# Optimization experiments

Hardware: AMD Instinct MI355X
Metric: run time of the kernel (lower is better)

## Reference

```python
import jax, jax.numpy as jnp
import numpy as np

HIDDEN = 1024
HEADS = 16
HEAD_DIM = HIDDEN // HEADS  # 64
LOCAL = (128, 128)
ROPE_MAX_POS = LOCAL[0] + LOCAL[1]  # 256 (local attention branch)
ROPE_BASE = 10000.0


def make_rope_cache(max_len, dim, base):
    positions = jnp.arange(max_len, dtype=jnp.float32)
    theta = 1.0 / base ** (jnp.arange(0, dim, 2, dtype=jnp.float32) / dim)
    angles = jnp.einsum('i,j->ij', positions, theta)
    return jnp.stack([jnp.cos(angles), jnp.sin(angles)], axis=-1)  # (max_len, dim//2, 2)


def apply_rope(x, cache):
    # x: (B, S, H, D); cache: (max_pos, D//2, 2)
    S = x.shape[1]
    pos = jnp.arange(S) % cache.shape[0]
    rc = cache[pos][None, :, None, :, :]  # (1, S, 1, D//2, 2)
    xr = x.reshape(*x.shape[:-1], -1, 2)
    x0, x1 = xr[..., 0], xr[..., 1]
    c, s = rc[..., 0], rc[..., 1]
    out = jnp.stack([x0 * c - x1 * s, x1 * c + x0 * s], axis=-1)
    return out.reshape(x.shape)


def sliding_window_mask(S, window, dtype):
    rel = jnp.arange(S)[:, None] - jnp.arange(S)[None, :]
    inside = (rel >= -window[0]) & (rel <= window[1])
    return jnp.where(inside, jnp.zeros((), dtype), -jnp.inf)[None, None]  # (1,1,S,S)


def setup_inputs() -> dict:
    key = jax.random.key(0)
    k1, k2, k3, k4, k5 = jax.random.split(key, 5)
    B, S = 2, 2048
    hidden_states = jax.random.normal(k1, (B, S, HIDDEN), dtype=jnp.float32)
    Wqkv_kernel = jax.random.normal(k2, (HIDDEN, 3 * HIDDEN), dtype=jnp.float32) / np.sqrt(HIDDEN)
    Wqkv_bias = jnp.zeros((3 * HIDDEN,), dtype=jnp.float32)
    Wo_kernel = jax.random.normal(k3, (HIDDEN, HIDDEN), dtype=jnp.float32) / np.sqrt(HIDDEN)
    Wo_bias = jnp.zeros((HIDDEN,), dtype=jnp.float32)
    rope_cache = make_rope_cache(ROPE_MAX_POS, HEAD_DIM, ROPE_BASE)
    return {
        'hidden_states': hidden_states,
        'Wqkv_kernel': Wqkv_kernel,
        'Wqkv_bias': Wqkv_bias,
        'Wo_kernel': Wo_kernel,
        'Wo_bias': Wo_bias,
        'rope_cache': rope_cache,
    }


def reference(hidden_states, Wqkv_kernel, Wqkv_bias, Wo_kernel, Wo_bias, rope_cache):
    B, S, _ = hidden_states.shape
    qkv = hidden_states @ Wqkv_kernel + Wqkv_bias  # (B,S,3*HIDDEN)
    qkv = qkv.reshape(B, S, 3, HEADS, HEAD_DIM)
    q = qkv[:, :, 0]  # (B,S,H,D)
    k = qkv[:, :, 1]
    v = qkv[:, :, 2]
    q = apply_rope(q, rope_cache)
    k = apply_rope(k, rope_cache)
    # to (B,H,S,D)
    q = jnp.transpose(q, (0, 2, 1, 3))
    k = jnp.transpose(k, (0, 2, 1, 3))
    v = jnp.transpose(v, (0, 2, 1, 3))
    scale = jnp.sqrt(jnp.float32(HEAD_DIM))
    scores = jnp.einsum('bhqd,bhkd->bhqk', q, k) / scale
    mask = sliding_window_mask(S, LOCAL, scores.dtype)
    probs = jax.nn.softmax(scores + mask, axis=-1)
    out = jnp.einsum('bhqk,bhkd->bqhd', probs, v).reshape(B, S, HIDDEN)
    out = out @ Wo_kernel + Wo_bias
    return out
```

## Files before the change

kernel.cpp:

```cpp
#include <hip/hip_runtime.h>
#include <hip/hip_bf16.h>

typedef __bf16 bf16x8 __attribute__((ext_vector_type(8)));
typedef __bf16 bf16x4 __attribute__((ext_vector_type(4)));
typedef float f32x4 __attribute__((ext_vector_type(4)));

#define SLEN 2048
#define NHEADS 16
#define HDIM 64

__global__ __launch_bounds__(256) void prep(const float* __restrict__ hidden,
                                            const float* __restrict__ Wqkv,
                                            const float* __restrict__ Wo,
                                            __bf16* __restrict__ A1,
                                            __bf16* __restrict__ Wt,
                                            __bf16* __restrict__ Wot) {
    int b = blockIdx.x;
    if (b < 4096) {
        int i = b * 256 + threadIdx.x;
        float4 v = reinterpret_cast<const float4*>(hidden)[i];
        bf16x4 o = { (__bf16)v.x, (__bf16)v.y, (__bf16)v.z, (__bf16)v.w };
        reinterpret_cast<bf16x4*>(A1)[i] = o;
    } else {
        __shared__ float tile[32][33];
        const float* W; __bf16* Dst; int N, bx, by;
        if (b < 7168) { int bb = b - 4096; W = Wqkv; Dst = Wt;  N = 3072; bx = bb % 96; by = bb / 96; }
        else          { int bb = b - 7168; W = Wo;   Dst = Wot; N = 1024; bx = bb % 32; by = bb / 32; }
        int tx = threadIdx.x & 31, ty = threadIdx.x >> 5;
        int n0 = bx * 32, k0 = by * 32;
        #pragma unroll
        for (int i = ty; i < 32; i += 8)
            tile[i][tx] = W[(size_t)(k0 + i) * N + n0 + tx];
        __syncthreads();
        #pragma unroll
        for (int i = ty; i < 32; i += 8)
            Dst[(size_t)(n0 + i) * 1024 + k0 + tx] = (__bf16)tile[tx][i];
    }
}

template <int TN>
__global__ __launch_bounds__(256) void gemm_bt(const __bf16* __restrict__ A,
                                               const __bf16* __restrict__ Bt,
                                               const float* __restrict__ bias,
                                               float* __restrict__ Cf,
                                               __bf16* __restrict__ Cq,
                                               __bf16* __restrict__ Ck,
                                               __bf16* __restrict__ Cv,
                                               int M, int N, int K, int epi) {
    constexpr int JN = TN / 32;
    __shared__ __align__(16) __bf16 As[128 * 40];
    __shared__ __align__(16) __bf16 Bs[TN * 40];

    int nb = N / TN;
    int bx = blockIdx.x % nb;
    int by = blockIdx.x / nb;
    int row0 = by * 128, col0 = bx * TN;

    int tid = threadIdx.x;
    int wave = tid >> 6, lane = tid & 63;
    int quad = lane >> 4, lrow = lane & 15;
    int wm = wave >> 1, wn = wave & 1;

    int r1 = tid >> 2;
    int kk = (tid & 3) * 8;
    const __bf16* Aptr = A + (size_t)(row0 + r1) * K + kk;
    const __bf16* Bptr = Bt + (size_t)(col0 + r1) * K + kk;

    f32x4 acc[4][JN];
    f32x4 zero = {0.f, 0.f, 0.f, 0.f};
    #pragma unroll
    for (int i = 0; i < 4; i++)
        #pragma unroll
        for (int j = 0; j < JN; j++) acc[i][j] = zero;

    for (int k0 = 0; k0 < K; k0 += 32) {
        bf16x8 a0 = *reinterpret_cast<const bf16x8*>(Aptr + k0);
        bf16x8 a1 = *reinterpret_cast<const bf16x8*>(Aptr + (size_t)64 * K + k0);
        bf16x8 b0 = *reinterpret_cast<const bf16x8*>(Bptr + k0);
        bf16x8 b1;
        if (TN == 128) b1 = *reinterpret_cast<const bf16x8*>(Bptr + (size_t)64 * K + k0);
        __syncthreads();
        *reinterpret_cast<bf16x8*>(&As[r1 * 40 + kk]) = a0;
        *reinterpret_cast<bf16x8*>(&As[(r1 + 64) * 40 + kk]) = a1;
        *reinterpret_cast<bf16x8*>(&Bs[r1 * 40 + kk]) = b0;
        if (TN == 128) *reinterpret_cast<bf16x8*>(&Bs[(r1 + 64) * 40 + kk]) = b1;
        __syncthreads();

        bf16x8 af[4], bfr[JN];
        #pragma unroll
        for (int i = 0; i < 4; i++)
            af[i] = *reinterpret_cast<const bf16x8*>(&As[(wm * 64 + i * 16 + lrow) * 40 + quad * 8]);
        #pragma unroll
        for (int j = 0; j < JN; j++)
            bfr[j] = *reinterpret_cast<const bf16x8*>(&Bs[(wn * (TN / 2) + j * 16 + lrow) * 40 + quad * 8]);
        #pragma unroll
        for (int i = 0; i < 4; i++)
            #pragma unroll
            for (int j = 0; j < JN; j++)
                acc[i][j] = __builtin_amdgcn_mfma_f32_16x16x32_bf16(af[i], bfr[j], acc[i][j], 0, 0, 0);
    }

    int part = col0 >> 10;
    #pragma unroll
    for (int i = 0; i < 4; i++) {
        int rowb = row0 + wm * 64 + i * 16 + quad * 4;
        #pragma unroll
        for (int j = 0; j < JN; j++) {
            int col = col0 + wn * (TN / 2) + j * 16 + lrow;
            float bsv = bias[col];
            #pragma unroll
            for (int r = 0; r < 4; r++) {
                int row = rowb + r;
                float v = acc[i][j][r] + bsv;
                if (epi == 0) {
                    Cf[(size_t)row * N + col] = v;
                } else {
                    int h = (col >> 6) & 15;
                    int d = col & 63;
                    int b = row >> 11;
                    int s = row & 2047;
                    __bf16* dst = (part == 0) ? Cq : ((part == 1) ? Ck : Cv);
                    dst[((size_t)(b * NHEADS + h) * SLEN + s) * HDIM + d] = (__bf16)v;
                }
            }
        }
    }
}

__global__ __launch_bounds__(256) void rope_kernel(__bf16* __restrict__ Q,
                                                   __bf16* __restrict__ K,
                                                   const float* __restrict__ rope) {
    int idx = blockIdx.x * 256 + threadIdx.x;
    int p = idx & 31;
    int s = (idx >> 5) & 2047;
    int bh = idx >> 16;
    size_t off = ((size_t)bh * SLEN + s) * HDIM + 2 * p;
    int pos = s & 255;
    float c = rope[(pos * 32 + p) * 2];
    float sn = rope[(pos * 32 + p) * 2 + 1];
    float q0 = (float)Q[off], q1 = (float)Q[off + 1];
    Q[off]     = (__bf16)(q0 * c - q1 * sn);
    Q[off + 1] = (__bf16)(q1 * c + q0 * sn);
    float k0 = (float)K[off], k1 = (float)K[off + 1];
    K[off]     = (__bf16)(k0 * c - k1 * sn);
    K[off + 1] = (__bf16)(k1 * c + k0 * sn);
}

__global__ __launch_bounds__(256) void attn_kernel(const __bf16* __restrict__ Q,
                                                   const __bf16* __restrict__ K,
                                                   const __bf16* __restrict__ V,
                                                   __bf16* __restrict__ O) {
    __shared__ __align__(16) __bf16 Vt[64][328];
    __shared__ __align__(16) __bf16 Pl[4][16][40];

    int qt = blockIdx.x & 31;
    int bh = blockIdx.x >> 5;
    int q0 = qt * 64;
    int kbase0 = q0 - 128;
    const __bf16* Qbh = Q + (size_t)bh * SLEN * HDIM;
    const __bf16* Kbh = K + (size_t)bh * SLEN * HDIM;
    const __bf16* Vbh = V + (size_t)bh * SLEN * HDIM;

    int tid = threadIdx.x;
    int wave = tid >> 6, lane = tid & 63;
    int quad = lane >> 4, lrow = lane & 15;
    int wq0 = q0 + wave * 16;

    {
        int dchunk = wave * 16;
        #pragma unroll
        for (int k = 0; k < 5; k++) {
            int off = k * 64 + lane;
            int krow = kbase0 + off;
            krow = min(max(krow, 0), SLEN - 1);
            const __bf16* vp = Vbh + (size_t)krow * HDIM + dchunk;
            bf16x8 v0 = *reinterpret_cast<const bf16x8*>(vp);
            bf16x8 v1 = *reinterpret_cast<const bf16x8*>(vp + 8);
            #pragma unroll
            for (int i = 0; i < 8; i++) {
                Vt[dchunk + i][off] = v0[i];
                Vt[dchunk + 8 + i][off] = v1[i];
            }
        }
    }

    bf16x8 qb0 = *reinterpret_cast<const bf16x8*>(Qbh + (size_t)(wq0 + lrow) * HDIM + quad * 8);
    bf16x8 qb1 = *reinterpret_cast<const bf16x8*>(Qbh + (size_t)(wq0 + lrow) * HDIM + 32 + quad * 8);

    __syncthreads();

    f32x4 zero = {0.f, 0.f, 0.f, 0.f};
    f32x4 acc[4], acc_l = zero;
    #pragma unroll
    for (int t = 0; t < 4; t++) acc[t] = zero;

    bf16x8 ones = { (__bf16)1.f, (__bf16)1.f, (__bf16)1.f, (__bf16)1.f,
                    (__bf16)1.f, (__bf16)1.f, (__bf16)1.f, (__bf16)1.f };

    int cbeg = wave >> 1;
    if (q0 < 128) { int e = (128 - q0) >> 5; if (e > cbeg) cbeg = e; }
    int cend = (16 * wave + 271) >> 5;
    { int e = (2175 - q0) >> 5; if (e < cend) cend = e; }

    auto loadK = [&](int c, bf16x8 kf[2][2]) {
        int kb = kbase0 + c * 32;
        #pragma unroll
        for (int sub = 0; sub < 2; sub++) {
            int kr = kb + sub * 16 + lrow;
            int krc = min(max(kr, 0), SLEN - 1);
            const __bf16* kp = Kbh + (size_t)krc * HDIM;
            kf[sub][0] = *reinterpret_cast<const bf16x8*>(kp + quad * 8);
            kf[sub][1] = *reinterpret_cast<const bf16x8*>(kp + 32 + quad * 8);
        }
    };

    bf16x8 ka[2][2];
    loadK(cbeg, ka);

    for (int c = cbeg; c <= cend; c++) {
        bf16x8 kn[2][2];
        if (c < cend) loadK(c + 1, kn);

        int kb = kbase0 + c * 32;
        int loc = c * 32;

        f32x4 st[2];
        #pragma unroll
        for (int sub = 0; sub < 2; sub++) {
            st[sub] = __builtin_amdgcn_mfma_f32_16x16x32_bf16(ka[sub][0], qb0, zero, 0, 0, 0);
            st[sub] = __builtin_amdgcn_mfma_f32_16x16x32_bf16(ka[sub][1], qb1, st[sub], 0, 0, 0);
        }

        int q = wq0 + lrow;
        #pragma unroll
        for (int sub = 0; sub < 2; sub++) {
            bf16x4 pk;
            #pragma unroll
            for (int r = 0; r < 4; r++) {
                int key = kb + sub * 16 + quad * 4 + r;
                int rel = key - q;
                bool valid = (rel >= -128) && (rel <= 128) && (key >= 0) && (key < SLEN);
                float p = valid ? __expf(st[sub][r] * 0.125f) : 0.0f;
                pk[r] = (__bf16)p;
            }
            *reinterpret_cast<bf16x4*>(&Pl[wave][lrow][sub * 16 + quad * 4]) = pk;
        }
        asm volatile("s_waitcnt lgkmcnt(0)" ::: "memory");

        bf16x8 bp = *reinterpret_cast<const bf16x8*>(&Pl[wave][lrow][quad * 8]);
        acc_l = __builtin_amdgcn_mfma_f32_16x16x32_bf16(ones, bp, acc_l, 0, 0, 0);
        #pragma unroll
        for (int t = 0; t < 4; t++) {
            bf16x8 va = *reinterpret_cast<const bf16x8*>(&Vt[t * 16 + lrow][loc + quad * 8]);
            acc[t] = __builtin_amdgcn_mfma_f32_16x16x32_bf16(va, bp, acc[t], 0, 0, 0);
        }

        #pragma unroll
        for (int sub = 0; sub < 2; sub++) {
            ka[sub][0] = kn[sub][0];
            ka[sub][1] = kn[sub][1];
        }
    }

    float inv = 1.0f / acc_l[0];
    int b = bh >> 4, h = bh & 15;
    int q = wq0 + lrow;
    size_t base = ((size_t)b * SLEN + q) * 1024 + h * HDIM;
    #pragma unroll
    for (int t = 0; t < 4; t++) {
        bf16x4 o;
        #pragma unroll
        for (int r = 0; r < 4; r++) o[r] = (__bf16)(acc[t][r] * inv);
        *reinterpret_cast<bf16x4*>(&O[base + t * 16 + quad * 4]) = o;
    }
}

extern "C" void kernel_launch(void* const* d_in, const int* in_sizes, int n_in,
                              void* d_out, int out_size, void* d_ws, size_t ws_size,
                              hipStream_t stream) {
    const float* hidden = (const float*)d_in[0];
    const float* Wqkv   = (const float*)d_in[1];
    const float* bqkv   = (const float*)d_in[2];
    const float* Wo     = (const float*)d_in[3];
    const float* bo     = (const float*)d_in[4];
    const float* rope   = (const float*)d_in[5];
    float* out = (float*)d_out;

    char* ws = (char*)d_ws;
    __bf16* A1  = (__bf16*)(ws);
    __bf16* Wt  = (__bf16*)(ws + 8388608);
    __bf16* Wot = (__bf16*)(ws + 14680064);
    __bf16* Qb  = (__bf16*)(ws + 16777216);
    __bf16* Kb  = (__bf16*)(ws + 25165824);
    __bf16* Vb  = (__bf16*)(ws + 33554432);
    __bf16* AO  = (__bf16*)(ws + 41943040);

    prep<<<8192, 256, 0, stream>>>(hidden, Wqkv, Wo, A1, Wt, Wot);

    gemm_bt<128><<<32 * 24, 256, 0, stream>>>(A1, Wt, bqkv, nullptr, Qb, Kb, Vb,
                                              4096, 3072, 1024, 1);
    rope_kernel<<<8192, 256, 0, stream>>>(Qb, Kb, rope);
    attn_kernel<<<1024, 256, 0, stream>>>(Qb, Kb, Vb, AO);
    gemm_bt<64><<<32 * 16, 256, 0, stream>>>(AO, Wot, bo, out, nullptr, nullptr, nullptr,
                                             4096, 1024, 1024, 0);
}
```

Baseline: 190.3 us.

## Double-buffer GEMM shared tiles and fuse fp32-to-bf16 cast of activations into GEMM

The GEMM kernel now keeps two LDS buffers. It prefetches the next K-slice into registers while the MFMAs run on the current slice, so each iteration needs one barrier instead of two. Separately, the hidden-state fp32-to-bf16 conversion is removed from the prep kernel and done inside the QKV GEMM's A-tile loads, which avoids writing and re-reading an 8 MB bf16 copy. In exchange, LDS use doubles, the fp32 A reads are twice as wide, and activations are converted redundantly across the 24 column blocks.

```diff
diff --git a/kernel.cpp b/kernel.cpp
--- a/kernel.cpp
+++ b/kernel.cpp
@@ -9,37 +9,28 @@
 #define NHEADS 16
 #define HDIM 64
 
-__global__ __launch_bounds__(256) void prep(const float* __restrict__ hidden,
-                                            const float* __restrict__ Wqkv,
+__global__ __launch_bounds__(256) void prep(const float* __restrict__ Wqkv,
                                             const float* __restrict__ Wo,
-                                            __bf16* __restrict__ A1,
                                             __bf16* __restrict__ Wt,
                                             __bf16* __restrict__ Wot) {
     int b = blockIdx.x;
-    if (b < 4096) {
-        int i = b * 256 + threadIdx.x;
-        float4 v = reinterpret_cast<const float4*>(hidden)[i];
-        bf16x4 o = { (__bf16)v.x, (__bf16)v.y, (__bf16)v.z, (__bf16)v.w };
-        reinterpret_cast<bf16x4*>(A1)[i] = o;
-    } else {
-        __shared__ float tile[32][33];
-        const float* W; __bf16* Dst; int N, bx, by;
-        if (b < 7168) { int bb = b - 4096; W = Wqkv; Dst = Wt;  N = 3072; bx = bb % 96; by = bb / 96; }
-        else          { int bb = b - 7168; W = Wo;   Dst = Wot; N = 1024; bx = bb % 32; by = bb / 32; }
-        int tx = threadIdx.x & 31, ty = threadIdx.x >> 5;
-        int n0 = bx * 32, k0 = by * 32;
-        #pragma unroll
-        for (int i = ty; i < 32; i += 8)
-            tile[i][tx] = W[(size_t)(k0 + i) * N + n0 + tx];
-        __syncthreads();
-        #pragma unroll
-        for (int i = ty; i < 32; i += 8)
-            Dst[(size_t)(n0 + i) * 1024 + k0 + tx] = (__bf16)tile[tx][i];
-    }
-}
-
-template <int TN>
-__global__ __launch_bounds__(256) void gemm_bt(const __bf16* __restrict__ A,
+    __shared__ float tile[32][33];
+    const float* W; __bf16* Dst; int N, bx, by;
+    if (b < 3072) { W = Wqkv; Dst = Wt;  N = 3072; bx = b % 96; by = b / 96; }
+    else          { int bb = b - 3072; W = Wo; Dst = Wot; N = 1024; bx = bb % 32; by = bb / 32; }
+    int tx = threadIdx.x & 31, ty = threadIdx.x >> 5;
+    int n0 = bx * 32, k0 = by * 32;
+    #pragma unroll
+    for (int i = ty; i < 32; i += 8)
+        tile[i][tx] = W[(size_t)(k0 + i) * N + n0 + tx];
+    __syncthreads();
+    #pragma unroll
+    for (int i = ty; i < 32; i += 8)
+        Dst[(size_t)(n0 + i) * 1024 + k0 + tx] = (__bf16)tile[tx][i];
+}
+
+template <int TN, bool CASTA>
+__global__ __launch_bounds__(256) void gemm_bt(const void* __restrict__ Avp,
                                                const __bf16* __restrict__ Bt,
                                                const float* __restrict__ bias,
                                                float* __restrict__ Cf,
@@ -48,8 +39,11 @@
                                                __bf16* __restrict__ Cv,
                                                int M, int N, int K, int epi) {
     constexpr int JN = TN / 32;
-    __shared__ __align__(16) __bf16 As[128 * 40];
-    __shared__ __align__(16) __bf16 Bs[TN * 40];
+    __shared__ __align__(16) __bf16 As[2][128 * 40];
+    __shared__ __align__(16) __bf16 Bs[2][TN * 40];
+
+    const float*  Af = (const float*)Avp;
+    const __bf16* Ab = (const __bf16*)Avp;
 
     int nb = N / TN;
     int bx = blockIdx.x % nb;
@@ -63,8 +57,22 @@
 
     int r1 = tid >> 2;
     int kk = (tid & 3) * 8;
-    const __bf16* Aptr = A + (size_t)(row0 + r1) * K + kk;
-    const __bf16* Bptr = Bt + (size_t)(col0 + r1) * K + kk;
+
+    auto loadA = [&](int k0, int roff) -> bf16x8 {
+        if (CASTA) {
+            const float* ap = Af + (size_t)(row0 + r1 + roff) * K + k0 + kk;
+            float4 f0 = *reinterpret_cast<const float4*>(ap);
+            float4 f1 = *reinterpret_cast<const float4*>(ap + 4);
+            bf16x8 o = { (__bf16)f0.x, (__bf16)f0.y, (__bf16)f0.z, (__bf16)f0.w,
+                         (__bf16)f1.x, (__bf16)f1.y, (__bf16)f1.z, (__bf16)f1.w };
+            return o;
+        } else {
+            return *reinterpret_cast<const bf16x8*>(Ab + (size_t)(row0 + r1 + roff) * K + k0 + kk);
+        }
+    };
+    auto loadB = [&](int k0, int roff) -> bf16x8 {
+        return *reinterpret_cast<const bf16x8*>(Bt + (size_t)(col0 + r1 + roff) * K + k0 + kk);
+    };
 
     f32x4 acc[4][JN];
     f32x4 zero = {0.f, 0.f, 0.f, 0.f};
@@ -73,31 +81,46 @@
         #pragma unroll
         for (int j = 0; j < JN; j++) acc[i][j] = zero;
 
+    bf16x8 a0 = loadA(0, 0), a1 = loadA(0, 64);
+    bf16x8 b0 = loadB(0, 0), b1;
+    if (TN == 128) b1 = loadB(0, 64);
+    *reinterpret_cast<bf16x8*>(&As[0][r1 * 40 + kk]) = a0;
+    *reinterpret_cast<bf16x8*>(&As[0][(r1 + 64) * 40 + kk]) = a1;
+    *reinterpret_cast<bf16x8*>(&Bs[0][r1 * 40 + kk]) = b0;
+    if (TN == 128) *reinterpret_cast<bf16x8*>(&Bs[0][(r1 + 64) * 40 + kk]) = b1;
+    __syncthreads();
+
     for (int k0 = 0; k0 < K; k0 += 32) {
-        bf16x8 a0 = *reinterpret_cast<const bf16x8*>(Aptr + k0);
-        bf16x8 a1 = *reinterpret_cast<const bf16x8*>(Aptr + (size_t)64 * K + k0);
-        bf16x8 b0 = *reinterpret_cast<const bf16x8*>(Bptr + k0);
-        bf16x8 b1;
-        if (TN == 128) b1 = *reinterpret_cast<const bf16x8*>(Bptr + (size_t)64 * K + k0);
-        __syncthreads();
-        *reinterpret_cast<bf16x8*>(&As[r1 * 40 + kk]) = a0;
-        *reinterpret_cast<bf16x8*>(&As[(r1 + 64) * 40 + kk]) = a1;
-        *reinterpret_cast<bf16x8*>(&Bs[r1 * 40 + kk]) = b0;
-        if (TN == 128) *reinterpret_cast<bf16x8*>(&Bs[(r1 + 64) * 40 + kk]) = b1;
-        __syncthreads();
+        int p = (k0 >> 5) & 1;
+        bool more = (k0 + 32) < K;
+        if (more) {
+            a0 = loadA(k0 + 32, 0);
+            a1 = loadA(k0 + 32, 64);
+            b0 = loadB(k0 + 32, 0);
+            if (TN == 128) b1 = loadB(k0 + 32, 64);
+        }
 
         bf16x8 af[4], bfr[JN];
         #pragma unroll
         for (int i = 0; i < 4; i++)
-            af[i] = *reinterpret_cast<const bf16x8*>(&As[(wm * 64 + i * 16 + lrow) * 40 + quad * 8]);
+            af[i] = *reinterpret_cast<const bf16x8*>(&As[p][(wm * 64 + i * 16 + lrow) * 40 + quad * 8]);
         #pragma unroll
         for (int j = 0; j < JN; j++)
-            bfr[j] = *reinterpret_cast<const bf16x8*>(&Bs[(wn * (TN / 2) + j * 16 + lrow) * 40 + quad * 8]);
+            bfr[j] = *reinterpret_cast<const bf16x8*>(&Bs[p][(wn * (TN / 2) + j * 16 + lrow) * 40 + quad * 8]);
         #pragma unroll
         for (int i = 0; i < 4; i++)
             #pragma unroll
             for (int j = 0; j < JN; j++)
                 acc[i][j] = __builtin_amdgcn_mfma_f32_16x16x32_bf16(af[i], bfr[j], acc[i][j], 0, 0, 0);
+
+        if (more) {
+            int q = p ^ 1;
+            *reinterpret_cast<bf16x8*>(&As[q][r1 * 40 + kk]) = a0;
+            *reinterpret_cast<bf16x8*>(&As[q][(r1 + 64) * 40 + kk]) = a1;
+            *reinterpret_cast<bf16x8*>(&Bs[q][r1 * 40 + kk]) = b0;
+            if (TN == 128) *reinterpret_cast<bf16x8*>(&Bs[q][(r1 + 64) * 40 + kk]) = b1;
+            __syncthreads();
+        }
     }
 
     int part = col0 >> 10;
@@ -287,20 +310,19 @@
     float* out = (float*)d_out;
 
     char* ws = (char*)d_ws;
-    __bf16* A1  = (__bf16*)(ws);
-    __bf16* Wt  = (__bf16*)(ws + 8388608);
-    __bf16* Wot = (__bf16*)(ws + 14680064);
-    __bf16* Qb  = (__bf16*)(ws + 16777216);
-    __bf16* Kb  = (__bf16*)(ws + 25165824);
-    __bf16* Vb  = (__bf16*)(ws + 33554432);
-    __bf16* AO  = (__bf16*)(ws + 41943040);
-
-    prep<<<8192, 256, 0, stream>>>(hidden, Wqkv, Wo, A1, Wt, Wot);
-
-    gemm_bt<128><<<32 * 24, 256, 0, stream>>>(A1, Wt, bqkv, nullptr, Qb, Kb, Vb,
-                                              4096, 3072, 1024, 1);
+    __bf16* Wt  = (__bf16*)(ws);
+    __bf16* Wot = (__bf16*)(ws + 6291456);
+    __bf16* Qb  = (__bf16*)(ws + 8388608);
+    __bf16* Kb  = (__bf16*)(ws + 16777216);
+    __bf16* Vb  = (__bf16*)(ws + 25165824);
+    __bf16* AO  = (__bf16*)(ws + 33554432);
+
+    prep<<<4096, 256, 0, stream>>>(Wqkv, Wo, Wt, Wot);
+
+    gemm_bt<128, true><<<32 * 24, 256, 0, stream>>>(hidden, Wt, bqkv, nullptr, Qb, Kb, Vb,
+                                                    4096, 3072, 1024, 1);
     rope_kernel<<<8192, 256, 0, stream>>>(Qb, Kb, rope);
     attn_kernel<<<1024, 256, 0, stream>>>(Qb, Kb, Vb, AO);
-    gemm_bt<64><<<32 * 16, 256, 0, stream>>>(AO, Wot, bo, out, nullptr, nullptr, nullptr,
-                                             4096, 1024, 1024, 0);
-}
+    gemm_bt<64, false><<<32 * 16, 256, 0, stream>>>(AO, Wot, bo, out, nullptr, nullptr, nullptr,
+                                                    4096, 1024, 1024, 0);
+}
```

New measurement: 229.2 us. +20.4%, slower.

## Pre-pack weights into MFMA fragment layout and load B directly from global

Applied to the files above, without the earlier changes.

The weight prep kernel now writes the transposed bf16 weights in a fragment-major layout matching the MFMA B-operand lane order. The GEMM then loads B fragments straight from global memory into registers with one coalesced 16-byte load per fragment, dropping the B shared-memory tile and its stores and reads. This cuts LDS traffic and LDS footprint. The cost is that each wave fetches its B data separately from global memory, with no reuse across waves through LDS.

```diff
diff --git a/kernel.cpp b/kernel.cpp
--- a/kernel.cpp
+++ b/kernel.cpp
@@ -21,26 +21,45 @@
         float4 v = reinterpret_cast<const float4*>(hidden)[i];
         bf16x4 o = { (__bf16)v.x, (__bf16)v.y, (__bf16)v.z, (__bf16)v.w };
         reinterpret_cast<bf16x4*>(A1)[i] = o;
+        return;
+    }
+    __shared__ float tile[32][33];
+    const float* W; __bf16* Dst; int N, n0, kc, bx, wn, j0, JNv;
+    if (b < 7168) {
+        int bb = b - 4096;
+        int bx96 = bb % 96; kc = bb / 96;
+        W = Wqkv; Dst = Wt; N = 3072;
+        n0 = bx96 * 32;
+        bx = bx96 >> 2; wn = (bx96 >> 1) & 1; j0 = (bx96 & 1) * 2; JNv = 4;
     } else {
-        __shared__ float tile[32][33];
-        const float* W; __bf16* Dst; int N, bx, by;
-        if (b < 7168) { int bb = b - 4096; W = Wqkv; Dst = Wt;  N = 3072; bx = bb % 96; by = bb / 96; }
-        else          { int bb = b - 7168; W = Wo;   Dst = Wot; N = 1024; bx = bb % 32; by = bb / 32; }
-        int tx = threadIdx.x & 31, ty = threadIdx.x >> 5;
-        int n0 = bx * 32, k0 = by * 32;
-        #pragma unroll
-        for (int i = ty; i < 32; i += 8)
-            tile[i][tx] = W[(size_t)(k0 + i) * N + n0 + tx];
-        __syncthreads();
-        #pragma unroll
-        for (int i = ty; i < 32; i += 8)
-            Dst[(size_t)(n0 + i) * 1024 + k0 + tx] = (__bf16)tile[tx][i];
+        int bb = b - 7168;
+        int bx32 = bb % 32; kc = bb / 32;
+        W = Wo; Dst = Wot; N = 1024;
+        n0 = bx32 * 32;
+        bx = bx32 >> 1; wn = bx32 & 1; j0 = 0; JNv = 2;
+    }
+    int k0 = kc * 32;
+    int tx = threadIdx.x & 31, ty = threadIdx.x >> 5;
+    #pragma unroll
+    for (int i = ty; i < 32; i += 8)
+        tile[i][tx] = W[(size_t)(k0 + i) * N + n0 + tx];
+    __syncthreads();
+    if (threadIdx.x < 128) {
+        int jh = threadIdx.x >> 6;
+        int lane = threadIdx.x & 63;
+        int lrow = lane & 15, quad = lane >> 4;
+        bf16x8 val;
+        #pragma unroll
+        for (int i = 0; i < 8; i++)
+            val[i] = (__bf16)tile[quad * 8 + i][jh * 16 + lrow];
+        size_t idx = ((((size_t)(bx * 32 + kc) * 2 + wn) * JNv + (j0 + jh)) * 64 + lane);
+        *reinterpret_cast<bf16x8*>(Dst + idx * 8) = val;
     }
 }
 
 template <int TN>
 __global__ __launch_bounds__(256) void gemm_bt(const __bf16* __restrict__ A,
-                                               const __bf16* __restrict__ Bt,
+                                               const __bf16* __restrict__ Bfrag,
                                                const float* __restrict__ bias,
                                                float* __restrict__ Cf,
                                                __bf16* __restrict__ Cq,
@@ -49,7 +68,6 @@
                                                int M, int N, int K, int epi) {
     constexpr int JN = TN / 32;
     __shared__ __align__(16) __bf16 As[128 * 40];
-    __shared__ __align__(16) __bf16 Bs[TN * 40];
 
     int nb = N / TN;
     int bx = blockIdx.x % nb;
@@ -64,7 +82,8 @@
     int r1 = tid >> 2;
     int kk = (tid & 3) * 8;
     const __bf16* Aptr = A + (size_t)(row0 + r1) * K + kk;
-    const __bf16* Bptr = Bt + (size_t)(col0 + r1) * K + kk;
+
+    const __bf16* Bbase = Bfrag + ((size_t)(bx * 32) * 2 + wn) * JN * 512 + (size_t)lane * 8;
 
     f32x4 acc[4][JN];
     f32x4 zero = {0.f, 0.f, 0.f, 0.f};
@@ -73,26 +92,24 @@
         #pragma unroll
         for (int j = 0; j < JN; j++) acc[i][j] = zero;
 
-    for (int k0 = 0; k0 < K; k0 += 32) {
+    int nkc = K >> 5;
+    for (int kc = 0; kc < nkc; kc++) {
+        int k0 = kc * 32;
         bf16x8 a0 = *reinterpret_cast<const bf16x8*>(Aptr + k0);
         bf16x8 a1 = *reinterpret_cast<const bf16x8*>(Aptr + (size_t)64 * K + k0);
-        bf16x8 b0 = *reinterpret_cast<const bf16x8*>(Bptr + k0);
-        bf16x8 b1;
-        if (TN == 128) b1 = *reinterpret_cast<const bf16x8*>(Bptr + (size_t)64 * K + k0);
+        bf16x8 bfr[JN];
+        #pragma unroll
+        for (int j = 0; j < JN; j++)
+            bfr[j] = *reinterpret_cast<const bf16x8*>(Bbase + (size_t)kc * JN * 1024 + j * 512);
         __syncthreads();
         *reinterpret_cast<bf16x8*>(&As[r1 * 40 + kk]) = a0;
         *reinterpret_cast<bf16x8*>(&As[(r1 + 64) * 40 + kk]) = a1;
-        *reinterpret_cast<bf16x8*>(&Bs[r1 * 40 + kk]) = b0;
-        if (TN == 128) *reinterpret_cast<bf16x8*>(&Bs[(r1 + 64) * 40 + kk]) = b1;
         __syncthreads();
 
-        bf16x8 af[4], bfr[JN];
+        bf16x8 af[4];
         #pragma unroll
         for (int i = 0; i < 4; i++)
             af[i] = *reinterpret_cast<const bf16x8*>(&As[(wm * 64 + i * 16 + lrow) * 40 + quad * 8]);
-        #pragma unroll
-        for (int j = 0; j < JN; j++)
-            bfr[j] = *reinterpret_cast<const bf16x8*>(&Bs[(wn * (TN / 2) + j * 16 + lrow) * 40 + quad * 8]);
         #pragma unroll
         for (int i = 0; i < 4; i++)
             #pragma unroll
```

New measurement: 184.9 us. 2.9% less time.
